# Kernel tuning notes

Hardware: AMD Instinct MI355X
Metric: run time of the kernel (lower is better)

The kernel has to match this reference:

```python
import jax, jax.numpy as jnp
import numpy as np

NH = 12      # bert-base heads
NL = 32      # num_latents
K = 64       # hard-coded topk in forward


def _ln(x, g, b):
    m = x.mean(-1, keepdims=True)
    v = ((x - m) ** 2).mean(-1, keepdims=True)
    return (x - m) / jnp.sqrt(v + 1e-12) * g + b


def _attn(xq, xkv, w, b, mask_add=None):
    # w: [4,H,H] (q,k,v,o), b: [4,H]
    B, Lq, H = xq.shape
    dh = H // NH
    q = (xq @ w[0] + b[0]).reshape(B, Lq, NH, dh)
    k = (xkv @ w[1] + b[1]).reshape(B, -1, NH, dh)
    v = (xkv @ w[2] + b[2]).reshape(B, -1, NH, dh)
    s = jnp.einsum('bqhd,bkhd->bhqk', q, k) / np.sqrt(dh).astype(xq.dtype)
    if mask_add is not None:
        s = s + mask_add
    p = jax.nn.softmax(s, axis=-1)          # [B,NH,Lq,Lk]
    o = jnp.einsum('bhqk,bkhd->bqhd', p, v).reshape(B, Lq, H)
    return o @ w[3] + b[3], p


def _cross_block(q, enc, w, b, g, lb, mask_add=None):
    # w:[L,8,H,H]; per layer: self-attn+LN then cross-attn+LN (FFN stripped)
    p_last = None
    for l in range(w.shape[0]):
        a, _ = _attn(q, q, w[l, :4], b[l, :4])
        q = _ln(q + a, g[l, 0], lb[l, 0])
        a, p_last = _attn(q, enc, w[l, 4:], b[l, 4:], mask_add)
        q = _ln(q + a, g[l, 1], lb[l, 1])
    return q, p_last


def _self_block(q, w, b, g, lb):
    probs = []
    for l in range(w.shape[0]):
        a, p = _attn(q, q, w[l], b[l])
        q = _ln(q + a, g[l, 0], lb[l, 0])
        probs.append(p)
    return q, jnp.concatenate(probs, axis=1)  # concat over head dim like torch.concat(attentions, dim=1)


def setup_inputs() -> dict:
    key = jax.random.key(0)
    ks = jax.random.split(key, 24)
    B, S, T, H, L = 32, 1024, 64, 768, 2
    std = 0.02
    inp = {
        'audio_embeds': jax.random.normal(ks[0], (B, S, H), jnp.float32),
        'text_embeds': jax.random.normal(ks[1], (B, T, H), jnp.float32),
        'attention_mask': jnp.ones((B, T), jnp.int32),
        'audio_qt': jax.random.normal(ks[2], (1, NL, H), jnp.float32) * std,
        'text_qt': jax.random.normal(ks[3], (1, NL, H), jnp.float32) * std,
    }
    for i, pre in enumerate(['tm', 'am', 'mg']):
        inp[pre + '_w'] = jax.random.normal(ks[4 + i], (L, 8, H, H), jnp.float32) * std
        inp[pre + '_b'] = jnp.zeros((L, 8, H), jnp.float32)
        inp[pre + '_g'] = jnp.ones((L, 2, H), jnp.float32)
        inp[pre + '_lb'] = jnp.zeros((L, 2, H), jnp.float32)
    inp['sel_w'] = jax.random.normal(ks[8], (L, 4, H, H), jnp.float32) * std
    inp['sel_b'] = jnp.zeros((L, 4, H), jnp.float32)
    inp['sel_g'] = jnp.ones((L, 1, H), jnp.float32)
    inp['sel_lb'] = jnp.zeros((L, 1, H), jnp.float32)
    return inp


def reference(audio_embeds, text_embeds, audio_qt, text_qt,
              tm_w, tm_b, tm_g, tm_lb, am_w, am_b, am_g, am_lb,
              sel_w, sel_b, sel_g, sel_lb, mg_w, mg_b, mg_g, mg_lb,
              attention_mask):
    B, S, H = audio_embeds.shape
    mask_add = (1.0 - attention_mask.astype(audio_embeds.dtype))[:, None, None, :] * -1e4

    # text token merger
    latent_text, _ = _cross_block(jnp.broadcast_to(text_qt, (B, NL, H)), text_embeds,
                                  tm_w, tm_b, tm_g, tm_lb, mask_add)
    # audio token merger (capture last-layer cross-attn probs)
    latent_audio, cross_p = _cross_block(jnp.broadcast_to(audio_qt, (B, NL, H)), audio_embeds,
                                         am_w, am_b, am_g, am_lb)
    latent_attention_score = cross_p.mean(axis=1)          # [B,NL,S]

    latent = jnp.concatenate([latent_audio, latent_text], axis=1)  # [B,2NL,H]
    fused, attn_all = _self_block(latent, sel_w, sel_b, sel_g, sel_lb)  # attn_all [B,L*NH,2NL,2NL]
    aas = attn_all[:, :, :NL, NL:].mean(axis=1)            # [B,NL,NL]

    imp = jnp.einsum('bqk,bks->bqs', aas, latent_attention_score).mean(axis=1)  # [B,S]
    _, idx = jax.lax.top_k(imp, K)
    sorted_idx = jnp.sort(idx, axis=1)                     # [B,K]

    sel_mask = jnp.zeros((B, S), bool).at[jnp.arange(B)[:, None], sorted_idx].set(True)
    q_tokens = jnp.take_along_axis(audio_embeds, sorted_idx[..., None], axis=1)  # [B,K,H]
    unsel_idx = jnp.argsort(sel_mask, axis=1, stable=True)[:, :S - K]            # order-preserving
    kv_rest = jnp.take_along_axis(audio_embeds, unsel_idx[..., None], axis=1)    # [B,S-K,H]
    kv = jnp.concatenate([kv_rest, fused], axis=1)                               # [B,S,H]

    out, _ = _cross_block(q_tokens, kv, mg_w, mg_b, mg_g, mg_lb)
    return out
```

## Files before the change

kernel.cpp:

```cpp
#include <hip/hip_runtime.h>
#include <hip/hip_bf16.h>
#include <math.h>

namespace {
constexpr int kB = 32, kS = 1024, kT = 64, kH = 768, kNH = 12, kDH = 64;
constexpr int kNL = 32, kTopK = 64, kL = 2;
constexpr size_t kMat = (size_t)kH * kH;
}

typedef _Float16 half8 __attribute__((ext_vector_type(8)));
typedef float floatx4 __attribute__((ext_vector_type(4)));

#define AS1U(p) ((const __attribute__((address_space(1))) unsigned int*)(p))
#define AS3U(p) ((__attribute__((address_space(3))) unsigned int*)(p))

__device__ __forceinline__ void split_write(float v, _Float16* H, _Float16* L, size_t i) {
    _Float16 h = (_Float16)v;
    H[i] = h;
    L[i] = (_Float16)(v - (float)h);
}

template<int NP>
__global__ __launch_bounds__(256) void gemm16x(
    const _Float16* __restrict__ Ah_, const _Float16* __restrict__ Al_,
    const _Float16* __restrict__ Bh_, const _Float16* __restrict__ Bl_,
    const float* __restrict__ bias,
    _Float16* __restrict__ Oh, _Float16* __restrict__ Ol, int M)
{
    const int nwg = gridDim.x;
    const int bid = blockIdx.x;
    const int cpx = nwg >> 3;
    const int swz = (bid & 7) * cpx + (bid >> 3);
    const int xn = swz % 6;
    const int ym = swz / 6;
    if (ym * 128 >= M) return;

    constexpr int NPL = (NP == 3) ? 4 : 2;
    __shared__ _Float16 lds[NPL * 4096];
    const int tid = threadIdx.x;
    const int lane = tid & 63, wave = tid >> 6;
    const size_t rm = (size_t)ym * 128;
    const size_t cn = (size_t)xn * 128;
    const int wr = (wave >> 1) * 64, wc = (wave & 1) * 64;

    const int lrow = lane >> 2;
    const int lchunk = (lane & 3) ^ ((lane >> 3) & 3);
    const int q = lane >> 4;
    const int fr = lane & 15;
    const int rslot = q ^ ((fr >> 1) & 3);

    const _Float16* gsrc;
    _Float16* lbase;
    int jbase;
    if constexpr (NP == 3) {
        gsrc = (wave == 0) ? Ah_ + rm * kH : (wave == 1) ? Al_ + rm * kH
             : (wave == 2) ? Bh_ + cn * kH : Bl_ + cn * kH;
        lbase = &lds[wave * 4096];
        jbase = 0;
    } else {
        gsrc = (wave < 2) ? Ah_ + rm * kH : Bh_ + cn * kH;
        lbase = &lds[(wave >> 1) * 4096];
        jbase = (wave & 1) * 4;
    }
    constexpr int CPW = (NP == 3) ? 8 : 4;

    floatx4 acc[4][4] = {};
    for (int k0 = 0; k0 < kH; k0 += 32) {
        #pragma unroll
        for (int c = 0; c < CPW; ++c) {
            int j = jbase + c;
            const _Float16* src = gsrc + (size_t)(j * 16 + lrow) * kH + k0 + lchunk * 8;
            _Float16* dst = lbase + j * 512 + lane * 8;
            __builtin_amdgcn_global_load_lds(AS1U(src), AS3U(dst), 16, 0, 0);
        }
        __syncthreads();
        half8 ah[4], bh[4], al[4], bl[4];
        #pragma unroll
        for (int m = 0; m < 4; ++m) {
            int r = wr + m * 16 + fr;
            ah[m] = *(const half8*)&lds[r * 32 + rslot * 8];
            if constexpr (NP == 3) al[m] = *(const half8*)&lds[4096 + r * 32 + rslot * 8];
        }
        constexpr int pb = (NP == 3) ? 2 : 1;
        #pragma unroll
        for (int n = 0; n < 4; ++n) {
            int r = wc + n * 16 + fr;
            bh[n] = *(const half8*)&lds[pb * 4096 + r * 32 + rslot * 8];
            if constexpr (NP == 3) bl[n] = *(const half8*)&lds[3 * 4096 + r * 32 + rslot * 8];
        }
        #pragma unroll
        for (int m = 0; m < 4; ++m)
            #pragma unroll
            for (int n = 0; n < 4; ++n) {
                acc[m][n] = __builtin_amdgcn_mfma_f32_16x16x32_f16(ah[m], bh[n], acc[m][n], 0, 0, 0);
                if constexpr (NP == 3) {
                    acc[m][n] = __builtin_amdgcn_mfma_f32_16x16x32_f16(ah[m], bl[n], acc[m][n], 0, 0, 0);
                    acc[m][n] = __builtin_amdgcn_mfma_f32_16x16x32_f16(al[m], bh[n], acc[m][n], 0, 0, 0);
                }
            }
        __syncthreads();
    }
    #pragma unroll
    for (int m = 0; m < 4; ++m) {
        int row0 = wr + m * 16 + (lane >> 4) * 4;
        #pragma unroll
        for (int n = 0; n < 4; ++n) {
            int col = (int)cn + wc + n * 16 + fr;
            float bv = bias[col];
            #pragma unroll
            for (int j = 0; j < 4; ++j) {
                float v = acc[m][n][j] + bv;
                size_t oi = (rm + row0 + j) * (size_t)kH + col;
                _Float16 hh = (_Float16)v;
                Oh[oi] = hh;
                if constexpr (NP == 3) Ol[oi] = (_Float16)(v - (float)hh);
            }
        }
    }
}

template<int NP>
__global__ __launch_bounds__(256) void gemm16s(
    const _Float16* __restrict__ Aqh, const _Float16* __restrict__ Aql,
    const _Float16* __restrict__ Aeh, const _Float16* __restrict__ Ael,
    const _Float16* __restrict__ Whb, const _Float16* __restrict__ Wlb,
    const float* __restrict__ bias,
    _Float16* __restrict__ O0h, _Float16* __restrict__ O0l,
    _Float16* __restrict__ O1h, _Float16* __restrict__ O1l,
    _Float16* __restrict__ O2h, _Float16* __restrict__ O2l,
    int Mq, int Mk)
{
    const int z = blockIdx.z;
    const int M = (z == 0) ? Mq : Mk;
    if ((int)blockIdx.x * 64 >= M) return;
    const _Float16* Ah = (z == 0) ? Aqh : Aeh;
    const _Float16* Al = (z == 0) ? Aql : Ael;
    const _Float16* Bh = Whb + (size_t)z * kMat;
    const _Float16* Bl = Wlb + (size_t)z * kMat;
    const float* bz = bias + z * kH;
    _Float16* Oh = (z == 0) ? O0h : (z == 1) ? O1h : O2h;
    _Float16* Ol = (z == 0) ? O0l : (z == 1) ? O1l : O2l;

    constexpr int NPL = (NP == 3) ? 4 : 2;
    __shared__ _Float16 lds[NPL * 2048];
    const int tid = threadIdx.x;
    const int lane = tid & 63, wave = tid >> 6;
    const size_t rm = (size_t)blockIdx.x * 64;
    const size_t cn = (size_t)blockIdx.y * 64;
    const int wr = (wave >> 1) * 32, wc = (wave & 1) * 32;

    const int lrow = lane >> 2;
    const int lchunk = (lane & 3) ^ ((lane >> 3) & 3);
    const int q = lane >> 4;
    const int fr = lane & 15;
    const int rslot = q ^ ((fr >> 1) & 3);

    const _Float16* gsrc;
    _Float16* lbase;
    int jbase;
    if constexpr (NP == 3) {
        gsrc = (wave == 0) ? Ah + rm * kH : (wave == 1) ? Al + rm * kH
             : (wave == 2) ? Bh + cn * kH : Bl + cn * kH;
        lbase = &lds[wave * 2048];
        jbase = 0;
    } else {
        gsrc = (wave < 2) ? Ah + rm * kH : Bh + cn * kH;
        lbase = &lds[(wave >> 1) * 2048];
        jbase = (wave & 1) * 2;
    }
    constexpr int CPW = (NP == 3) ? 4 : 2;

    floatx4 acc[2][2] = {};
    for (int k0 = 0; k0 < kH; k0 += 32) {
        #pragma unroll
        for (int c = 0; c < CPW; ++c) {
            int j = jbase + c;
            const _Float16* src = gsrc + (size_t)(j * 16 + lrow) * kH + k0 + lchunk * 8;
            _Float16* dst = lbase + j * 512 + lane * 8;
            __builtin_amdgcn_global_load_lds(AS1U(src), AS3U(dst), 16, 0, 0);
        }
        __syncthreads();
        half8 ah[2], bh[2], al[2], bl[2];
        #pragma unroll
        for (int m = 0; m < 2; ++m) {
            int r = wr + m * 16 + fr;
            ah[m] = *(const half8*)&lds[r * 32 + rslot * 8];
            if constexpr (NP == 3) al[m] = *(const half8*)&lds[2048 + r * 32 + rslot * 8];
        }
        constexpr int pb = (NP == 3) ? 2 : 1;
        #pragma unroll
        for (int n = 0; n < 2; ++n) {
            int r = wc + n * 16 + fr;
            bh[n] = *(const half8*)&lds[pb * 2048 + r * 32 + rslot * 8];
            if constexpr (NP == 3) bl[n] = *(const half8*)&lds[3 * 2048 + r * 32 + rslot * 8];
        }
        #pragma unroll
        for (int m = 0; m < 2; ++m)
            #pragma unroll
            for (int n = 0; n < 2; ++n) {
                acc[m][n] = __builtin_amdgcn_mfma_f32_16x16x32_f16(ah[m], bh[n], acc[m][n], 0, 0, 0);
                if constexpr (NP == 3) {
                    acc[m][n] = __builtin_amdgcn_mfma_f32_16x16x32_f16(ah[m], bl[n], acc[m][n], 0, 0, 0);
                    acc[m][n] = __builtin_amdgcn_mfma_f32_16x16x32_f16(al[m], bh[n], acc[m][n], 0, 0, 0);
                }
            }
        __syncthreads();
    }
    #pragma unroll
    for (int m = 0; m < 2; ++m) {
        int row0 = wr + m * 16 + (lane >> 4) * 4;
        #pragma unroll
        for (int n = 0; n < 2; ++n) {
            int col = (int)cn + wc + n * 16 + fr;
            float bv = bz[col];
            #pragma unroll
            for (int j = 0; j < 4; ++j) {
                float v = acc[m][n][j] + bv;
                size_t oi = (rm + row0 + j) * (size_t)kH + col;
                _Float16 hh = (_Float16)v;
                Oh[oi] = hh;
                if constexpr (NP == 3) Ol[oi] = (_Float16)(v - (float)hh);
            }
        }
    }
}

template<int NP>
__global__ __launch_bounds__(256) void gemm_o32s(
    const _Float16* __restrict__ Ah_, const _Float16* __restrict__ Al_,
    const _Float16* __restrict__ Bh_, const _Float16* __restrict__ Bl_,
    const float* __restrict__ bias, float* __restrict__ Y, int M)
{
    constexpr int NPL = (NP == 3) ? 4 : 2;
    __shared__ _Float16 lds[NPL * 2048];
    const int tid = threadIdx.x;
    const int lane = tid & 63, wave = tid >> 6;
    const size_t rm = (size_t)blockIdx.x * 64;
    const size_t cn = (size_t)blockIdx.y * 64;
    const int wr = (wave >> 1) * 32, wc = (wave & 1) * 32;

    const int lrow = lane >> 2;
    const int lchunk = (lane & 3) ^ ((lane >> 3) & 3);
    const int q = lane >> 4;
    const int fr = lane & 15;
    const int rslot = q ^ ((fr >> 1) & 3);

    const _Float16* gsrc;
    _Float16* lbase;
    int jbase;
    if constexpr (NP == 3) {
        gsrc = (wave == 0) ? Ah_ + rm * kH : (wave == 1) ? Al_ + rm * kH
             : (wave == 2) ? Bh_ + cn * kH : Bl_ + cn * kH;
        lbase = &lds[wave * 2048];
        jbase = 0;
    } else {
        gsrc = (wave < 2) ? Ah_ + rm * kH : Bh_ + cn * kH;
        lbase = &lds[(wave >> 1) * 2048];
        jbase = (wave & 1) * 2;
    }
    constexpr int CPW = (NP == 3) ? 4 : 2;

    floatx4 acc[2][2] = {};
    for (int k0 = 0; k0 < kH; k0 += 32) {
        #pragma unroll
        for (int c = 0; c < CPW; ++c) {
            int j = jbase + c;
            const _Float16* src = gsrc + (size_t)(j * 16 + lrow) * kH + k0 + lchunk * 8;
            _Float16* dst = lbase + j * 512 + lane * 8;
            __builtin_amdgcn_global_load_lds(AS1U(src), AS3U(dst), 16, 0, 0);
        }
        __syncthreads();
        half8 ah[2], bh[2], al[2], bl[2];
        #pragma unroll
        for (int m = 0; m < 2; ++m) {
            int r = wr + m * 16 + fr;
            ah[m] = *(const half8*)&lds[r * 32 + rslot * 8];
            if constexpr (NP == 3) al[m] = *(const half8*)&lds[2048 + r * 32 + rslot * 8];
        }
        constexpr int pb = (NP == 3) ? 2 : 1;
        #pragma unroll
        for (int n = 0; n < 2; ++n) {
            int r = wc + n * 16 + fr;
            bh[n] = *(const half8*)&lds[pb * 2048 + r * 32 + rslot * 8];
            if constexpr (NP == 3) bl[n] = *(const half8*)&lds[3 * 2048 + r * 32 + rslot * 8];
        }
        #pragma unroll
        for (int m = 0; m < 2; ++m)
            #pragma unroll
            for (int n = 0; n < 2; ++n) {
                acc[m][n] = __builtin_amdgcn_mfma_f32_16x16x32_f16(ah[m], bh[n], acc[m][n], 0, 0, 0);
                if constexpr (NP == 3) {
                    acc[m][n] = __builtin_amdgcn_mfma_f32_16x16x32_f16(ah[m], bl[n], acc[m][n], 0, 0, 0);
                    acc[m][n] = __builtin_amdgcn_mfma_f32_16x16x32_f16(al[m], bh[n], acc[m][n], 0, 0, 0);
                }
            }
        __syncthreads();
    }
    #pragma unroll
    for (int m = 0; m < 2; ++m) {
        int row0 = wr + m * 16 + (lane >> 4) * 4;
        #pragma unroll
        for (int n = 0; n < 2; ++n) {
            int col = (int)cn + wc + n * 16 + fr;
            float bv = bias[col];
            #pragma unroll
            for (int j = 0; j < 4; ++j)
                Y[(rm + row0 + j) * (size_t)kH + col] = acc[m][n][j] + bv;
        }
    }
}

template<int NP>
__global__ __launch_bounds__(256) void attn_big(
    const _Float16* __restrict__ Qh, const _Float16* __restrict__ Ql,
    const _Float16* __restrict__ Kh, const _Float16* __restrict__ Kl,
    float* __restrict__ P, int Lq, int Lk)
{
    constexpr int NPL = (NP == 3) ? 2 : 1;
    const int tid = threadIdx.x, lane = tid & 63, wave = tid >> 6;
    const int fr = lane & 15, part = lane >> 4;
    const int bh = blockIdx.x, b = bh / kNH, h = bh % kNH;
    const int q0 = blockIdx.y * 32;
    const int key0 = wave * 256;
    __shared__ float red[32][4];

    half8 qa[2][2][NPL];
    #pragma unroll
    for (int m = 0; m < 2; ++m)
        #pragma unroll
        for (int c = 0; c < 2; ++c) {
            size_t ro = (size_t)(b * Lq + q0 + m * 16 + fr) * kH + h * kDH + c * 32 + part * 8;
            qa[m][c][0] = *(const half8*)&Qh[ro];
            if constexpr (NP == 3) qa[m][c][1] = *(const half8*)&Ql[ro];
        }
    floatx4 acc[2][16] = {};
    #pragma unroll
    for (int n = 0; n < 16; ++n)
        #pragma unroll
        for (int c = 0; c < 2; ++c) {
            size_t ro = (size_t)(b * Lk + key0 + n * 16 + fr) * kH + h * kDH + c * 32 + part * 8;
            half8 kh8 = *(const half8*)&Kh[ro];
            half8 kl8;
            if constexpr (NP == 3) kl8 = *(const half8*)&Kl[ro];
            #pragma unroll
            for (int m = 0; m < 2; ++m) {
                acc[m][n] = __builtin_amdgcn_mfma_f32_16x16x32_f16(qa[m][c][0], kh8, acc[m][n], 0, 0, 0);
                if constexpr (NP == 3) {
                    acc[m][n] = __builtin_amdgcn_mfma_f32_16x16x32_f16(qa[m][c][0], kl8, acc[m][n], 0, 0, 0);
                    acc[m][n] = __builtin_amdgcn_mfma_f32_16x16x32_f16(qa[m][c][1], kh8, acc[m][n], 0, 0, 0);
                }
            }
        }
    #pragma unroll
    for (int m = 0; m < 2; ++m)
        #pragma unroll
        for (int n = 0; n < 16; ++n)
            #pragma unroll
            for (int j = 0; j < 4; ++j) acc[m][n][j] *= 0.125f;
    #pragma unroll
    for (int m = 0; m < 2; ++m)
        #pragma unroll
        for (int j = 0; j < 4; ++j) {
            float v = acc[m][0][j];
            #pragma unroll
            for (int n = 1; n < 16; ++n) v = fmaxf(v, acc[m][n][j]);
            #pragma unroll
            for (int o = 1; o < 16; o <<= 1) v = fmaxf(v, __shfl_xor(v, o));
            red[m * 16 + part * 4 + j][wave] = v;
        }
    __syncthreads();
    float gm[2][4];
    #pragma unroll
    for (int m = 0; m < 2; ++m)
        #pragma unroll
        for (int j = 0; j < 4; ++j) {
            int r = m * 16 + part * 4 + j;
            gm[m][j] = fmaxf(fmaxf(red[r][0], red[r][1]), fmaxf(red[r][2], red[r][3]));
        }
    __syncthreads();
    #pragma unroll
    for (int m = 0; m < 2; ++m)
        #pragma unroll
        for (int j = 0; j < 4; ++j) {
            float s = 0.f;
            #pragma unroll
            for (int n = 0; n < 16; ++n) {
                float e = expf(acc[m][n][j] - gm[m][j]);
                acc[m][n][j] = e;
                s += e;
            }
            #pragma unroll
            for (int o = 1; o < 16; o <<= 1) s += __shfl_xor(s, o);
            red[m * 16 + part * 4 + j][wave] = s;
        }
    __syncthreads();
    #pragma unroll
    for (int m = 0; m < 2; ++m)
        #pragma unroll
        for (int j = 0; j < 4; ++j) {
            int r = m * 16 + part * 4 + j;
            float inv = 1.0f / (red[r][0] + red[r][1] + red[r][2] + red[r][3]);
            size_t rowbase = ((size_t)bh * Lq + q0 + m * 16 + part * 4 + j) * Lk + key0;
            #pragma unroll
            for (int n = 0; n < 16; ++n)
                P[rowbase + n * 16 + fr] = acc[m][n][j] * inv;
        }
}

template<int LQ, int NP>
__global__ __launch_bounds__((LQ / 16) * 64) void pv_mfma(
    const float* __restrict__ P,
    const _Float16* __restrict__ Vh, const _Float16* __restrict__ Vl,
    _Float16* __restrict__ Oh, _Float16* __restrict__ Ol, int Lk)
{
    constexpr int NW = LQ / 16, NT = NW * 64;
    constexpr int NPL = (NP == 3) ? 2 : 1;
    __shared__ _Float16 vT[NPL][64][72];
    const int tid = threadIdx.x, lane = tid & 63, wave = tid >> 6;
    const int fr = lane & 15, part = lane >> 4;
    const int bh = blockIdx.x, b = bh / kNH, h = bh % kNH;
    const int qbase = wave * 16;

    floatx4 acc[4] = {};
    for (int kb = 0; kb < Lk; kb += 64) {
        for (int idx = tid; idx < 64 * 8; idx += NT) {
            int r = idx >> 3, c8 = idx & 7;
            half8 v = *(const half8*)&Vh[(size_t)(b * Lk + kb + r) * kH + h * kDH + c8 * 8];
            #pragma unroll
            for (int e = 0; e < 8; ++e) vT[0][c8 * 8 + e][r] = v[e];
            if constexpr (NP == 3) {
                half8 w = *(const half8*)&Vl[(size_t)(b * Lk + kb + r) * kH + h * kDH + c8 * 8];
                #pragma unroll
                for (int e = 0; e < 8; ++e) vT[1][c8 * 8 + e][r] = w[e];
            }
        }
        __syncthreads();
        half8 pa[2][NPL];
        #pragma unroll
        for (int c = 0; c < 2; ++c) {
            const float* src = &P[((size_t)bh * LQ + qbase + fr) * Lk + kb + c * 32 + part * 8];
            float4 x = *(const float4*)src, y = *(const float4*)(src + 4);
            float vv[8] = {x.x, x.y, x.z, x.w, y.x, y.y, y.z, y.w};
            #pragma unroll
            for (int e = 0; e < 8; ++e) {
                _Float16 hh = (_Float16)vv[e];
                pa[c][0][e] = hh;
                if constexpr (NP == 3) pa[c][1][e] = (_Float16)(vv[e] - (float)hh);
            }
        }
        #pragma unroll
        for (int n = 0; n < 4; ++n)
            #pragma unroll
            for (int c = 0; c < 2; ++c) {
                half8 bh8 = *(const half8*)&vT[0][n * 16 + fr][c * 32 + part * 8];
                acc[n] = __builtin_amdgcn_mfma_f32_16x16x32_f16(pa[c][0], bh8, acc[n], 0, 0, 0);
                if constexpr (NP == 3) {
                    half8 bl8 = *(const half8*)&vT[1][n * 16 + fr][c * 32 + part * 8];
                    acc[n] = __builtin_amdgcn_mfma_f32_16x16x32_f16(pa[c][0], bl8, acc[n], 0, 0, 0);
                    acc[n] = __builtin_amdgcn_mfma_f32_16x16x32_f16(pa[c][1], bh8, acc[n], 0, 0, 0);
                }
            }
        __syncthreads();
    }
    #pragma unroll
    for (int n = 0; n < 4; ++n)
        #pragma unroll
        for (int j = 0; j < 4; ++j) {
            size_t oi = (size_t)(b * LQ + qbase + part * 4 + j) * kH + h * kDH + n * 16 + fr;
            float v = acc[n][j];
            _Float16 hh = (_Float16)v;
            Oh[oi] = hh;
            if constexpr (NP == 3) Ol[oi] = (_Float16)(v - (float)hh);
        }
}

template<int LQ, int LK, int NP, bool MASKED, bool CAPTURE>
__global__ __launch_bounds__((LQ / 16) * 64) void attn_small(
    const _Float16* Qh, const _Float16* Ql,
    const _Float16* __restrict__ Kh, const _Float16* __restrict__ Kl,
    const _Float16* __restrict__ Vh, const _Float16* __restrict__ Vl,
    _Float16* Oh, _Float16* Ol,
    float* __restrict__ Pcap, const int* __restrict__ amask)
{
    constexpr int NW = LQ / 16, NT = NW * 64, NN = LK / 16, NC = LK / 32;
    constexpr int NPL = (NP == 3) ? 2 : 1;
    constexpr int PIT = LK + 8;
    __shared__ _Float16 vT[NPL][64][PIT];
    __shared__ _Float16 Pld[NW][NPL][16][PIT];
    const int tid = threadIdx.x, lane = tid & 63, wave = tid >> 6;
    const int fr = lane & 15, part = lane >> 4;
    const int bh = blockIdx.x, b = bh / kNH, h = bh % kNH;

    for (int idx = tid; idx < LK * 8; idx += NT) {
        int r = idx >> 3, c8 = idx & 7;
        half8 v = *(const half8*)&Vh[(size_t)(b * LK + r) * kH + h * kDH + c8 * 8];
        #pragma unroll
        for (int e = 0; e < 8; ++e) vT[0][c8 * 8 + e][r] = v[e];
        if constexpr (NP == 3) {
            half8 w = *(const half8*)&Vl[(size_t)(b * LK + r) * kH + h * kDH + c8 * 8];
            #pragma unroll
            for (int e = 0; e < 8; ++e) vT[1][c8 * 8 + e][r] = w[e];
        }
    }
    half8 qa[2][NPL];
    #pragma unroll
    for (int c = 0; c < 2; ++c) {
        size_t ro = (size_t)(b * LQ + wave * 16 + fr) * kH + h * kDH + c * 32 + part * 8;
        qa[c][0] = *(const half8*)&Qh[ro];
        if constexpr (NP == 3) qa[c][1] = *(const half8*)&Ql[ro];
    }
    floatx4 acc[NN] = {};
    #pragma unroll
    for (int n = 0; n < NN; ++n)
        #pragma unroll
        for (int c = 0; c < 2; ++c) {
            size_t ro = (size_t)(b * LK + n * 16 + fr) * kH + h * kDH + c * 32 + part * 8;
            half8 kh8 = *(const half8*)&Kh[ro];
            acc[n] = __builtin_amdgcn_mfma_f32_16x16x32_f16(qa[c][0], kh8, acc[n], 0, 0, 0);
            if constexpr (NP == 3) {
                half8 kl8 = *(const half8*)&Kl[ro];
                acc[n] = __builtin_amdgcn_mfma_f32_16x16x32_f16(qa[c][0], kl8, acc[n], 0, 0, 0);
                acc[n] = __builtin_amdgcn_mfma_f32_16x16x32_f16(qa[c][1], kh8, acc[n], 0, 0, 0);
            }
        }
    #pragma unroll
    for (int n = 0; n < NN; ++n) {
        float madd = 0.f;
        if constexpr (MASKED)
            madd = (1.0f - (float)amask[b * kT + n * 16 + fr]) * -1e4f;
        #pragma unroll
        for (int j = 0; j < 4; ++j) acc[n][j] = acc[n][j] * 0.125f + madd;
    }
    #pragma unroll
    for (int j = 0; j < 4; ++j) {
        float m = acc[0][j];
        #pragma unroll
        for (int n = 1; n < NN; ++n) m = fmaxf(m, acc[n][j]);
        #pragma unroll
        for (int o = 1; o < 16; o <<= 1) m = fmaxf(m, __shfl_xor(m, o));
        float s = 0.f;
        #pragma unroll
        for (int n = 0; n < NN; ++n) { float e = expf(acc[n][j] - m); acc[n][j] = e; s += e; }
        #pragma unroll
        for (int o = 1; o < 16; o <<= 1) s += __shfl_xor(s, o);
        float inv = 1.0f / s;
        #pragma unroll
        for (int n = 0; n < NN; ++n) acc[n][j] *= inv;
    }
    #pragma unroll
    for (int n = 0; n < NN; ++n)
        #pragma unroll
        for (int j = 0; j < 4; ++j) {
            float p = acc[n][j];
            if constexpr (CAPTURE)
                Pcap[((size_t)bh * LQ + wave * 16 + part * 4 + j) * LK + n * 16 + fr] = p;
            _Float16 ph = (_Float16)p;
            Pld[wave][0][part * 4 + j][n * 16 + fr] = ph;
            if constexpr (NP == 3)
                Pld[wave][1][part * 4 + j][n * 16 + fr] = (_Float16)(p - (float)ph);
        }
    __syncthreads();
    floatx4 o4[4] = {};
    #pragma unroll
    for (int n = 0; n < 4; ++n)
        #pragma unroll
        for (int c = 0; c < NC; ++c) {
            half8 ph8 = *(const half8*)&Pld[wave][0][fr][c * 32 + part * 8];
            half8 vh8 = *(const half8*)&vT[0][n * 16 + fr][c * 32 + part * 8];
            o4[n] = __builtin_amdgcn_mfma_f32_16x16x32_f16(ph8, vh8, o4[n], 0, 0, 0);
            if constexpr (NP == 3) {
                half8 pl8 = *(const half8*)&Pld[wave][1][fr][c * 32 + part * 8];
                half8 vl8 = *(const half8*)&vT[1][n * 16 + fr][c * 32 + part * 8];
                o4[n] = __builtin_amdgcn_mfma_f32_16x16x32_f16(ph8, vl8, o4[n], 0, 0, 0);
                o4[n] = __builtin_amdgcn_mfma_f32_16x16x32_f16(pl8, vh8, o4[n], 0, 0, 0);
            }
        }
    #pragma unroll
    for (int n = 0; n < 4; ++n)
        #pragma unroll
        for (int j = 0; j < 4; ++j) {
            size_t oi = (size_t)(b * LQ + wave * 16 + part * 4 + j) * kH + h * kDH + n * 16 + fr;
            float v = o4[n][j];
            _Float16 hh = (_Float16)v;
            Oh[oi] = hh;
            if constexpr (NP == 3) Ol[oi] = (_Float16)(v - (float)hh);
        }
}

__global__ __launch_bounds__(256) void wconv(const float* __restrict__ W,
    _Float16* __restrict__ Th, _Float16* __restrict__ Tl)
{
    __shared__ float t[32][33];
    const int mat = blockIdx.z;
    const int k0 = blockIdx.y * 32, n0 = blockIdx.x * 32;
    const int tid = threadIdx.x;
    #pragma unroll
    for (int i = 0; i < 4; ++i) {
        int e = tid + i * 256, r = e >> 5, c = e & 31;
        t[r][c] = W[(size_t)mat * kMat + (size_t)(k0 + r) * kH + n0 + c];
    }
    __syncthreads();
    #pragma unroll
    for (int i = 0; i < 4; ++i) {
        int e = tid + i * 256, r = e >> 5, c = e & 31;
        float v = t[c][r];
        split_write(v, Th, Tl, (size_t)mat * kMat + (size_t)(n0 + r) * kH + k0 + c);
    }
}

__global__ __launch_bounds__(256) void split2(const float* __restrict__ X,
    _Float16* __restrict__ H, _Float16* __restrict__ L, int n)
{
    int i = (blockIdx.x * 256 + threadIdx.x) * 4;
    if (i >= n) return;
    float4 v = *(const float4*)&X[i];
    split_write(v.x, H, L, i);
    split_write(v.y, H, L, i + 1);
    split_write(v.z, H, L, i + 2);
    split_write(v.w, H, L, i + 3);
}

__global__ __launch_bounds__(256) void ln_residual(const float* __restrict__ X,
    const float* __restrict__ A, const float* __restrict__ g,
    const float* __restrict__ lb, float* __restrict__ Y,
    _Float16* __restrict__ Yh, _Float16* __restrict__ Yl)
{
    const size_t row = blockIdx.x;
    const int tid = threadIdx.x;
    __shared__ float red[4];
    float x[3];
    float sum = 0.f;
    #pragma unroll
    for (int i = 0; i < 3; ++i) {
        int c = tid + i * 256;
        x[i] = X[row * kH + c] + A[row * kH + c];
        sum += x[i];
    }
    for (int o = 32; o > 0; o >>= 1) sum += __shfl_xor(sum, o);
    if ((tid & 63) == 0) red[tid >> 6] = sum;
    __syncthreads();
    sum = red[0] + red[1] + red[2] + red[3];
    float mean = sum * (1.0f / 768.0f);
    float vs = 0.f;
    #pragma unroll
    for (int i = 0; i < 3; ++i) { float d = x[i] - mean; vs += d * d; }
    for (int o = 32; o > 0; o >>= 1) vs += __shfl_xor(vs, o);
    __syncthreads();
    if ((tid & 63) == 0) red[tid >> 6] = vs;
    __syncthreads();
    vs = red[0] + red[1] + red[2] + red[3];
    float inv = 1.0f / sqrtf(vs * (1.0f / 768.0f) + 1e-12f);
    #pragma unroll
    for (int i = 0; i < 3; ++i) {
        int c = tid + i * 256;
        float y = (x[i] - mean) * inv * g[c] + lb[c];
        Y[row * kH + c] = y;
        if (Yh) split_write(y, Yh, Yl, row * kH + c);
    }
}

__global__ __launch_bounds__(256) void mean_heads(const float* __restrict__ P,
    float* __restrict__ out)
{
    const int bq = blockIdx.x;
    const int b = bq / kNL, q = bq % kNL;
    for (int s = threadIdx.x; s < kS; s += 256) {
        float acc = 0.f;
        for (int h = 0; h < kNH; ++h)
            acc += P[((size_t)(b * kNH + h) * kNL + q) * kS + s];
        out[(size_t)bq * kS + s] = acc * (1.0f / kNH);
    }
}

__global__ __launch_bounds__(256) void aas_acc(const float* __restrict__ P,
    float* __restrict__ aas, int init)
{
    const int b = blockIdx.x;
    for (int idx = threadIdx.x; idx < kNL * kNL; idx += 256) {
        int q = idx >> 5, k = idx & 31;
        float acc = 0.f;
        for (int h = 0; h < kNH; ++h)
            acc += P[((size_t)(b * kNH + h) * 64 + q) * 64 + 32 + k];
        size_t o = (size_t)b * kNL * kNL + idx;
        if (init) aas[o] = acc; else aas[o] += acc;
    }
}

__global__ __launch_bounds__(256) void imp_kernel(const float* __restrict__ aas,
    const float* __restrict__ score, float* __restrict__ imp)
{
    const int b = blockIdx.x;
    __shared__ float w[kNL];
    if (threadIdx.x < kNL) {
        float acc = 0.f;
        for (int q = 0; q < kNL; ++q)
            acc += aas[((size_t)b * kNL + q) * kNL + threadIdx.x];
        w[threadIdx.x] = acc;
    }
    __syncthreads();
    for (int s = threadIdx.x; s < kS; s += 256) {
        float acc = 0.f;
        for (int k = 0; k < kNL; ++k)
            acc += w[k] * score[((size_t)b * kNL + k) * kS + s];
        imp[(size_t)b * kS + s] = acc;
    }
}

__global__ __launch_bounds__(256) void topk_kernel(const float* __restrict__ imp,
    int* __restrict__ selidx, int* __restrict__ unselidx)
{
    const int b = blockIdx.x;
    const int tid = threadIdx.x;
    __shared__ unsigned long long keys[kS];
    __shared__ int wsum[4];
    for (int i = tid; i < kS; i += 256) {
        unsigned u = __float_as_uint(imp[(size_t)b * kS + i]);
        u = (u & 0x80000000u) ? ~u : (u | 0x80000000u);
        keys[i] = ((unsigned long long)u << 32) | (unsigned)(kS - 1 - i);
    }
    __syncthreads();
    unsigned long long me[4];
    int r[4] = {0, 0, 0, 0};
    #pragma unroll
    for (int j = 0; j < 4; ++j) me[j] = keys[tid * 4 + j];
    for (int t = 0; t < kS; ++t) {
        unsigned long long k = keys[t];
        #pragma unroll
        for (int j = 0; j < 4; ++j) r[j] += (k > me[j]) ? 1 : 0;
    }
    int flag[4], cnt = 0;
    #pragma unroll
    for (int j = 0; j < 4; ++j) { flag[j] = (r[j] < kTopK); cnt += flag[j]; }
    const int lane = tid & 63, w = tid >> 6;
    int incl = cnt;
    for (int o = 1; o < 64; o <<= 1) {
        int t = __shfl_up(incl, o);
        if (lane >= o) incl += t;
    }
    if (lane == 63) wsum[w] = incl;
    __syncthreads();
    int wbase = 0;
    for (int i = 0; i < w; ++i) wbase += wsum[i];
    int sbase = wbase + incl - cnt;
    int ubase = tid * 4 - sbase;
    #pragma unroll
    for (int j = 0; j < 4; ++j) {
        int i = tid * 4 + j;
        if (flag[j]) selidx[b * kTopK + sbase++] = i;
        else         unselidx[b * (kS - kTopK) + ubase++] = i;
    }
}

__global__ __launch_bounds__(256) void bcast_q(const float* __restrict__ qt,
    float* __restrict__ q, _Float16* __restrict__ Qh, _Float16* __restrict__ Ql)
{
    const int bn = blockIdx.x;
    const int n = bn & (kNL - 1);
    for (int c = threadIdx.x; c < kH; c += 256) {
        float v = qt[(size_t)n * kH + c];
        q[(size_t)bn * kH + c] = v;
        split_write(v, Qh, Ql, (size_t)bn * kH + c);
    }
}

__global__ __launch_bounds__(256) void concat_lat(const float* __restrict__ qa,
    const float* __restrict__ qt, float* __restrict__ lat,
    _Float16* __restrict__ Lh, _Float16* __restrict__ Ll)
{
    const int br = blockIdx.x;
    const int b = br >> 6, r = br & 63;
    const float* src = (r < kNL) ? qa + (size_t)(b * kNL + r) * kH
                                 : qt + (size_t)(b * kNL + (r - kNL)) * kH;
    for (int c = threadIdx.x; c < kH; c += 256) {
        float v = src[c];
        lat[(size_t)br * kH + c] = v;
        split_write(v, Lh, Ll, (size_t)br * kH + c);
    }
}

__global__ __launch_bounds__(256) void gather_q(const float* __restrict__ audio,
    const int* __restrict__ selidx, float* __restrict__ qm,
    _Float16* __restrict__ Qh, _Float16* __restrict__ Ql)
{
    const int bj = blockIdx.x;
    const int b = bj >> 6;
    const int srow = selidx[bj];
    const float* src = audio + ((size_t)b * kS + srow) * kH;
    for (int c = threadIdx.x; c < kH; c += 256) {
        float v = src[c];
        qm[(size_t)bj * kH + c] = v;
        split_write(v, Qh, Ql, (size_t)bj * kH + c);
    }
}

__global__ __launch_bounds__(256) void build_kv(const float* __restrict__ audio,
    const float* __restrict__ fused, const int* __restrict__ unselidx,
    _Float16* __restrict__ Kh, _Float16* __restrict__ Kl)
{
    const int br = blockIdx.x;
    const int b = br >> 10, r = br & 1023;
    const float* src;
    if (r < kS - kTopK) src = audio + ((size_t)b * kS + unselidx[b * (kS - kTopK) + r]) * kH;
    else                src = fused + (size_t)(b * kTopK + (r - (kS - kTopK))) * kH;
    for (int c = threadIdx.x; c < kH; c += 256)
        split_write(src[c], Kh, Kl, (size_t)br * kH + c);
}

extern "C" void kernel_launch(void* const* d_in, const int* in_sizes, int n_in,
                              void* d_out, int out_size, void* d_ws, size_t ws_size,
                              hipStream_t stream)
{
    const float* audio    = (const float*)d_in[0];
    const float* text     = (const float*)d_in[1];
    const int*   amask    = (const int*)  d_in[2];
    const float* audio_qt = (const float*)d_in[3];
    const float* text_qt  = (const float*)d_in[4];
    const float* tm_w  = (const float*)d_in[5];
    const float* tm_b  = (const float*)d_in[6];
    const float* tm_g  = (const float*)d_in[7];
    const float* tm_lb = (const float*)d_in[8];
    const float* am_w  = (const float*)d_in[9];
    const float* am_b  = (const float*)d_in[10];
    const float* am_g  = (const float*)d_in[11];
    const float* am_lb = (const float*)d_in[12];
    const float* mg_w  = (const float*)d_in[13];
    const float* mg_b  = (const float*)d_in[14];
    const float* mg_g  = (const float*)d_in[15];
    const float* mg_lb = (const float*)d_in[16];
    const float* sel_w  = (const float*)d_in[17];
    const float* sel_b  = (const float*)d_in[18];
    const float* sel_g  = (const float*)d_in[19];
    const float* sel_lb = (const float*)d_in[20];
    (void)in_sizes; (void)n_in; (void)out_size;

    char* base = (char*)d_ws;
    size_t off = 0;
    auto A = [&](size_t bytes) {
        off = (off + 255) & ~(size_t)255;
        void* p = base + off; off += bytes; return p;
    };
    float* Pbuf   = (float*)A((size_t)kB * kNH * 64 * kS * 4);
    float* attA   = (float*)A((size_t)2048 * kH * 4);
    float* q_text = (float*)A((size_t)1024 * kH * 4);
    float* q_audio= (float*)A((size_t)1024 * kH * 4);
    float* latent = (float*)A((size_t)2048 * kH * 4);
    float* qmerge = (float*)A((size_t)2048 * kH * 4);
    float* latsc  = (float*)A((size_t)kB * kNL * kS * 4);
    float* aas    = (float*)A((size_t)kB * kNL * kNL * 4);
    float* impb   = (float*)A((size_t)kB * kS * 4);
    int* selidx   = (int*)A((size_t)kB * kTopK * 4);
    int* unselidx = (int*)A((size_t)kB * (kS - kTopK) * 4);
    _Float16* Wh  = (_Float16*)A(8 * kMat * 2);
    _Float16* Wl  = (_Float16*)A(8 * kMat * 2);
    _Float16* BGh = (_Float16*)A((size_t)kB * kS * kH * 2);
    _Float16* BGl = (_Float16*)A((size_t)kB * kS * kH * 2);
    _Float16* PTh = (_Float16*)A((size_t)kB * kT * kH * 2);
    _Float16* PTl = (_Float16*)A((size_t)kB * kT * kH * 2);
    _Float16* PLqh= (_Float16*)A((size_t)2048 * kH * 2);
    _Float16* PLql= (_Float16*)A((size_t)2048 * kH * 2);
    _Float16* PLoh= (_Float16*)A((size_t)2048 * kH * 2);
    _Float16* PLol= (_Float16*)A((size_t)2048 * kH * 2);
    _Float16* KVh = (_Float16*)A((size_t)kB * kS * kH * 2);
    _Float16* KVl = (_Float16*)A((size_t)kB * kS * kH * 2);
    if (off > ws_size) return;

    _Float16* Qh = PLoh;
    _Float16* Ql = PLol;

    auto attn = [&](const float* qf, int Lq,
                    const _Float16* qah, const _Float16* qal,
                    const _Float16* eah, const _Float16* eal, int Lk,
                    int wmat, const float* bias, const float* g, const float* lb,
                    const int* mask, int capture, bool np3,
                    float* q_out, _Float16* oh, _Float16* ol)
    {
        const int Mq = kB * Lq, Mk = kB * Lk;
        const _Float16* WhB = Wh + (size_t)wmat * kMat;
        const _Float16* WlB = Wl + (size_t)wmat * kMat;
        if (Lk >= 256) {
            dim3 gq(Mq / 64, 12, 1);
            if (np3) gemm16s<3><<<gq, 256, 0, stream>>>(qah, qal, qah, qal, WhB, WlB, bias,
                         Qh, Ql, nullptr, nullptr, nullptr, nullptr, Mq, Mq);
            else     gemm16s<1><<<gq, 256, 0, stream>>>(qah, qal, qah, qal, WhB, WlB, bias,
                         Qh, Ql, nullptr, nullptr, nullptr, nullptr, Mq, Mq);
            const int nwgK = 6 * (Mk / 128);
            if (np3) gemm16x<3><<<nwgK, 256, 0, stream>>>(eah, eal, WhB + 1 * kMat, WlB + 1 * kMat,
                         bias + 1 * kH, KVh, KVl, Mk);
            else     gemm16x<1><<<nwgK, 256, 0, stream>>>(eah, eal, WhB + 1 * kMat, WlB + 1 * kMat,
                         bias + 1 * kH, KVh, KVl, Mk);
            dim3 g2(kB * kNH, Lq / 32);
            if (np3) attn_big<3><<<g2, 256, 0, stream>>>(Qh, Ql, KVh, KVl, Pbuf, Lq, Lk);
            else     attn_big<1><<<g2, 256, 0, stream>>>(Qh, Ql, KVh, KVl, Pbuf, Lq, Lk);
            if (capture == 1) mean_heads<<<kB * kNL, 256, 0, stream>>>(Pbuf, latsc);
            if (np3) gemm16x<3><<<nwgK, 256, 0, stream>>>(eah, eal, WhB + 2 * kMat, WlB + 2 * kMat,
                         bias + 2 * kH, KVh, KVl, Mk);
            else     gemm16x<1><<<nwgK, 256, 0, stream>>>(eah, eal, WhB + 2 * kMat, WlB + 2 * kMat,
                         bias + 2 * kH, KVh, KVl, Mk);
            if (Lq == 32) {
                if (np3) pv_mfma<32, 3><<<kB * kNH, 128, 0, stream>>>(Pbuf, KVh, KVl, PLoh, PLol, Lk);
                else     pv_mfma<32, 1><<<kB * kNH, 128, 0, stream>>>(Pbuf, KVh, KVl, PLoh, PLol, Lk);
            } else {
                if (np3) pv_mfma<64, 3><<<kB * kNH, 256, 0, stream>>>(Pbuf, KVh, KVl, PLoh, PLol, Lk);
                else     pv_mfma<64, 1><<<kB * kNH, 256, 0, stream>>>(Pbuf, KVh, KVl, PLoh, PLol, Lk);
            }
        } else {
            _Float16* V2h = KVh + (size_t)Mk * kH;
            _Float16* V2l = KVl + (size_t)Mk * kH;
            const int gx = (Mq > Mk ? Mq : Mk) / 64;
            dim3 g1(gx, 12, 3);
            if (np3) gemm16s<3><<<g1, 256, 0, stream>>>(qah, qal, eah, eal, WhB, WlB, bias,
                         Qh, Ql, KVh, KVl, V2h, V2l, Mq, Mk);
            else     gemm16s<1><<<g1, 256, 0, stream>>>(qah, qal, eah, eal, WhB, WlB, bias,
                         Qh, Ql, KVh, KVl, V2h, V2l, Mq, Mk);
            if (Lq == 32 && Lk == 32)
                attn_small<32, 32, 3, false, false><<<kB * kNH, 128, 0, stream>>>(
                    Qh, Ql, KVh, KVl, V2h, V2l, PLoh, PLol, nullptr, nullptr);
            else if (Lq == 32 && Lk == 64)
                attn_small<32, 64, 3, true, false><<<kB * kNH, 128, 0, stream>>>(
                    Qh, Ql, KVh, KVl, V2h, V2l, PLoh, PLol, nullptr, mask);
            else if (np3)
                attn_small<64, 64, 3, false, true><<<kB * kNH, 256, 0, stream>>>(
                    Qh, Ql, KVh, KVl, V2h, V2l, PLoh, PLol, Pbuf, nullptr);
            else
                attn_small<64, 64, 1, false, false><<<kB * kNH, 256, 0, stream>>>(
                    Qh, Ql, KVh, KVl, V2h, V2l, PLoh, PLol, nullptr, nullptr);
            if (capture == 2)      aas_acc<<<kB, 256, 0, stream>>>(Pbuf, aas, 1);
            else if (capture == 3) aas_acc<<<kB, 256, 0, stream>>>(Pbuf, aas, 0);
        }
        dim3 g4(Mq / 64, 12);
        if (np3) gemm_o32s<3><<<g4, 256, 0, stream>>>(PLoh, PLol, WhB + 3 * kMat, WlB + 3 * kMat,
                     bias + 3 * kH, attA, Mq);
        else     gemm_o32s<1><<<g4, 256, 0, stream>>>(PLoh, PLol, WhB + 3 * kMat, WlB + 3 * kMat,
                     bias + 3 * kH, attA, Mq);
        ln_residual<<<Mq, 256, 0, stream>>>(qf, attA, g, lb, q_out, oh, ol);
    };

    split2<<<(kB * kT * kH) / 1024, 256, 0, stream>>>(text, PTh, PTl, kB * kT * kH);
    split2<<<(kB * kS * kH) / 1024, 256, 0, stream>>>(audio, BGh, BGl, kB * kS * kH);

    bcast_q<<<kB * kNL, 256, 0, stream>>>(text_qt, q_text, PLqh, PLql);
    for (int l = 0; l < kL; ++l) {
        wconv<<<dim3(24, 24, 8), 256, 0, stream>>>(tm_w + (size_t)l * 8 * kMat, Wh, Wl);
        attn(q_text, kNL, PLqh, PLql, PLqh, PLql, kNL, 0,
             tm_b + (size_t)l * 8 * kH, tm_g + (size_t)l * 2 * kH, tm_lb + (size_t)l * 2 * kH,
             nullptr, 0, true, q_text, PLqh, PLql);
        attn(q_text, kNL, PLqh, PLql, PTh, PTl, kT, 4,
             tm_b + ((size_t)l * 8 + 4) * kH, tm_g + ((size_t)l * 2 + 1) * kH, tm_lb + ((size_t)l * 2 + 1) * kH,
             amask, 0, true, q_text, PLqh, PLql);
    }
    bcast_q<<<kB * kNL, 256, 0, stream>>>(audio_qt, q_audio, PLqh, PLql);
    for (int l = 0; l < kL; ++l) {
        wconv<<<dim3(24, 24, 8), 256, 0, stream>>>(am_w + (size_t)l * 8 * kMat, Wh, Wl);
        attn(q_audio, kNL, PLqh, PLql, PLqh, PLql, kNL, 0,
             am_b + (size_t)l * 8 * kH, am_g + (size_t)l * 2 * kH, am_lb + (size_t)l * 2 * kH,
             nullptr, 0, true, q_audio, PLqh, PLql);
        attn(q_audio, kNL, PLqh, PLql, BGh, BGl, kS, 4,
             am_b + ((size_t)l * 8 + 4) * kH, am_g + ((size_t)l * 2 + 1) * kH, am_lb + ((size_t)l * 2 + 1) * kH,
             nullptr, (l == kL - 1) ? 1 : 0, true, q_audio, PLqh, PLql);
    }
    concat_lat<<<kB * 64, 256, 0, stream>>>(q_audio, q_text, latent, PLqh, PLql);
    for (int l = 0; l < kL; ++l) {
        wconv<<<dim3(24, 24, 4), 256, 0, stream>>>(sel_w + (size_t)l * 4 * kMat, Wh, Wl);
        attn(latent, 64, PLqh, PLql, PLqh, PLql, 64, 0,
             sel_b + (size_t)l * 4 * kH, sel_g + (size_t)l * kH, sel_lb + (size_t)l * kH,
             nullptr, (l == 0) ? 2 : 3, true, latent, PLqh, PLql);
    }
    imp_kernel<<<kB, 256, 0, stream>>>(aas, latsc, impb);
    topk_kernel<<<kB, 256, 0, stream>>>(impb, selidx, unselidx);
    gather_q<<<kB * kTopK, 256, 0, stream>>>(audio, selidx, qmerge, PLqh, PLql);
    build_kv<<<kB * kS, 256, 0, stream>>>(audio, latent, unselidx, BGh, BGl);
    for (int l = 0; l < kL; ++l) {
        wconv<<<dim3(24, 24, 8), 256, 0, stream>>>(mg_w + (size_t)l * 8 * kMat, Wh, Wl);
        attn(qmerge, 64, PLqh, PLql, PLqh, PLql, 64, 0,
             mg_b + (size_t)l * 8 * kH, mg_g + (size_t)l * 2 * kH, mg_lb + (size_t)l * 2 * kH,
             nullptr, 0, false, qmerge, PLqh, PLql);
        float* qo = (l == kL - 1) ? (float*)d_out : qmerge;
        _Float16* oh = (l == kL - 1) ? nullptr : PLqh;
        _Float16* ol = (l == kL - 1) ? nullptr : PLql;
        attn(qmerge, 64, PLqh, PLql, BGh, BGl, kS, 4,
             mg_b + ((size_t)l * 8 + 4) * kH, mg_g + ((size_t)l * 2 + 1) * kH, mg_lb + ((size_t)l * 2 + 1) * kH,
             nullptr, 0, false, qo, oh, ol);
    }
}
```

Before: 2.088 ms.

## Double-buffer LDS tiles in GEMM kernels to overlap loads with MFMA

The three split-fp16 GEMM kernels now keep two LDS buffers. Each iteration issues the global-to-LDS copy for the next K tile before running the MFMAs on the current one, and the trailing barrier per iteration is removed. The aim is to hide global memory latency behind the matrix math and to halve the barrier count. In exchange, LDS use per block doubles (64KB for the large 3-plane variant), which can lower occupancy.

Measured after the change: 2.016 ms (median of 2 runs). 3.4% less time.

```diff
diff --git a/kernel.cpp b/kernel.cpp
--- a/kernel.cpp
+++ b/kernel.cpp
@@ -36,7 +36,7 @@
     if (ym * 128 >= M) return;
 
     constexpr int NPL = (NP == 3) ? 4 : 2;
-    __shared__ _Float16 lds[NPL * 4096];
+    __shared__ _Float16 lds[2][NPL * 4096];
     const int tid = threadIdx.x;
     const int lane = tid & 63, wave = tid >> 6;
     const size_t rm = (size_t)ym * 128;
@@ -50,43 +50,50 @@
     const int rslot = q ^ ((fr >> 1) & 3);
 
     const _Float16* gsrc;
-    _Float16* lbase;
-    int jbase;
+    int lplane, jbase;
     if constexpr (NP == 3) {
         gsrc = (wave == 0) ? Ah_ + rm * kH : (wave == 1) ? Al_ + rm * kH
              : (wave == 2) ? Bh_ + cn * kH : Bl_ + cn * kH;
-        lbase = &lds[wave * 4096];
+        lplane = wave;
         jbase = 0;
     } else {
         gsrc = (wave < 2) ? Ah_ + rm * kH : Bh_ + cn * kH;
-        lbase = &lds[(wave >> 1) * 4096];
+        lplane = wave >> 1;
         jbase = (wave & 1) * 4;
     }
     constexpr int CPW = (NP == 3) ? 8 : 4;
 
-    floatx4 acc[4][4] = {};
-    for (int k0 = 0; k0 < kH; k0 += 32) {
+    auto stage = [&](int buf, int k0) {
         #pragma unroll
         for (int c = 0; c < CPW; ++c) {
             int j = jbase + c;
             const _Float16* src = gsrc + (size_t)(j * 16 + lrow) * kH + k0 + lchunk * 8;
-            _Float16* dst = lbase + j * 512 + lane * 8;
+            _Float16* dst = &lds[buf][lplane * 4096 + j * 512 + lane * 8];
             __builtin_amdgcn_global_load_lds(AS1U(src), AS3U(dst), 16, 0, 0);
         }
+    };
+
+    floatx4 acc[4][4] = {};
+    int cur = 0;
+    stage(0, 0);
+    constexpr int NT = kH / 32;
+    for (int kt = 0; kt < NT; ++kt) {
         __syncthreads();
+        if (kt + 1 < NT) stage(cur ^ 1, (kt + 1) * 32);
+        const _Float16* L = lds[cur];
         half8 ah[4], bh[4], al[4], bl[4];
         #pragma unroll
         for (int m = 0; m < 4; ++m) {
             int r = wr + m * 16 + fr;
-            ah[m] = *(const half8*)&lds[r * 32 + rslot * 8];
-            if constexpr (NP == 3) al[m] = *(const half8*)&lds[4096 + r * 32 + rslot * 8];
+            ah[m] = *(const half8*)&L[r * 32 + rslot * 8];
+            if constexpr (NP == 3) al[m] = *(const half8*)&L[4096 + r * 32 + rslot * 8];
         }
         constexpr int pb = (NP == 3) ? 2 : 1;
         #pragma unroll
         for (int n = 0; n < 4; ++n) {
             int r = wc + n * 16 + fr;
-            bh[n] = *(const half8*)&lds[pb * 4096 + r * 32 + rslot * 8];
-            if constexpr (NP == 3) bl[n] = *(const half8*)&lds[3 * 4096 + r * 32 + rslot * 8];
+            bh[n] = *(const half8*)&L[pb * 4096 + r * 32 + rslot * 8];
+            if constexpr (NP == 3) bl[n] = *(const half8*)&L[3 * 4096 + r * 32 + rslot * 8];
         }
         #pragma unroll
         for (int m = 0; m < 4; ++m)
@@ -98,7 +105,7 @@
                     acc[m][n] = __builtin_amdgcn_mfma_f32_16x16x32_f16(al[m], bh[n], acc[m][n], 0, 0, 0);
                 }
             }
-        __syncthreads();
+        cur ^= 1;
     }
     #pragma unroll
     for (int m = 0; m < 4; ++m) {
@@ -142,7 +149,7 @@
     _Float16* Ol = (z == 0) ? O0l : (z == 1) ? O1l : O2l;
 
     constexpr int NPL = (NP == 3) ? 4 : 2;
-    __shared__ _Float16 lds[NPL * 2048];
+    __shared__ _Float16 lds[2][NPL * 2048];
     const int tid = threadIdx.x;
     const int lane = tid & 63, wave = tid >> 6;
     const size_t rm = (size_t)blockIdx.x * 64;
@@ -156,43 +163,50 @@
     const int rslot = q ^ ((fr >> 1) & 3);
 
     const _Float16* gsrc;
-    _Float16* lbase;
-    int jbase;
+    int lplane, jbase;
     if constexpr (NP == 3) {
         gsrc = (wave == 0) ? Ah + rm * kH : (wave == 1) ? Al + rm * kH
              : (wave == 2) ? Bh + cn * kH : Bl + cn * kH;
-        lbase = &lds[wave * 2048];
+        lplane = wave;
         jbase = 0;
     } else {
         gsrc = (wave < 2) ? Ah + rm * kH : Bh + cn * kH;
-        lbase = &lds[(wave >> 1) * 2048];
+        lplane = wave >> 1;
         jbase = (wave & 1) * 2;
     }
     constexpr int CPW = (NP == 3) ? 4 : 2;
 
-    floatx4 acc[2][2] = {};
-    for (int k0 = 0; k0 < kH; k0 += 32) {
+    auto stage = [&](int buf, int k0) {
         #pragma unroll
         for (int c = 0; c < CPW; ++c) {
             int j = jbase + c;
             const _Float16* src = gsrc + (size_t)(j * 16 + lrow) * kH + k0 + lchunk * 8;
-            _Float16* dst = lbase + j * 512 + lane * 8;
+            _Float16* dst = &lds[buf][lplane * 2048 + j * 512 + lane * 8];
             __builtin_amdgcn_global_load_lds(AS1U(src), AS3U(dst), 16, 0, 0);
         }
+    };
+
+    floatx4 acc[2][2] = {};
+    int cur = 0;
+    stage(0, 0);
+    constexpr int NT = kH / 32;
+    for (int kt = 0; kt < NT; ++kt) {
         __syncthreads();
+        if (kt + 1 < NT) stage(cur ^ 1, (kt + 1) * 32);
+        const _Float16* L = lds[cur];
         half8 ah[2], bh[2], al[2], bl[2];
         #pragma unroll
         for (int m = 0; m < 2; ++m) {
             int r = wr + m * 16 + fr;
-            ah[m] = *(const half8*)&lds[r * 32 + rslot * 8];
-            if constexpr (NP == 3) al[m] = *(const half8*)&lds[2048 + r * 32 + rslot * 8];
+            ah[m] = *(const half8*)&L[r * 32 + rslot * 8];
+            if constexpr (NP == 3) al[m] = *(const half8*)&L[2048 + r * 32 + rslot * 8];
         }
         constexpr int pb = (NP == 3) ? 2 : 1;
         #pragma unroll
         for (int n = 0; n < 2; ++n) {
             int r = wc + n * 16 + fr;
-            bh[n] = *(const half8*)&lds[pb * 2048 + r * 32 + rslot * 8];
-            if constexpr (NP == 3) bl[n] = *(const half8*)&lds[3 * 2048 + r * 32 + rslot * 8];
+            bh[n] = *(const half8*)&L[pb * 2048 + r * 32 + rslot * 8];
+            if constexpr (NP == 3) bl[n] = *(const half8*)&L[3 * 2048 + r * 32 + rslot * 8];
         }
         #pragma unroll
         for (int m = 0; m < 2; ++m)
@@ -204,7 +218,7 @@
                     acc[m][n] = __builtin_amdgcn_mfma_f32_16x16x32_f16(al[m], bh[n], acc[m][n], 0, 0, 0);
                 }
             }
-        __syncthreads();
+        cur ^= 1;
     }
     #pragma unroll
     for (int m = 0; m < 2; ++m) {
@@ -232,7 +246,7 @@
     const float* __restrict__ bias, float* __restrict__ Y, int M)
 {
     constexpr int NPL = (NP == 3) ? 4 : 2;
-    __shared__ _Float16 lds[NPL * 2048];
+    __shared__ _Float16 lds[2][NPL * 2048];
     const int tid = threadIdx.x;
     const int lane = tid & 63, wave = tid >> 6;
     const size_t rm = (size_t)blockIdx.x * 64;
@@ -246,43 +260,50 @@
     const int rslot = q ^ ((fr >> 1) & 3);
 
     const _Float16* gsrc;
-    _Float16* lbase;
-    int jbase;
+    int lplane, jbase;
     if constexpr (NP == 3) {
         gsrc = (wave == 0) ? Ah_ + rm * kH : (wave == 1) ? Al_ + rm * kH
              : (wave == 2) ? Bh_ + cn * kH : Bl_ + cn * kH;
-        lbase = &lds[wave * 2048];
+        lplane = wave;
         jbase = 0;
     } else {
         gsrc = (wave < 2) ? Ah_ + rm * kH : Bh_ + cn * kH;
-        lbase = &lds[(wave >> 1) * 2048];
+        lplane = wave >> 1;
         jbase = (wave & 1) * 2;
     }
     constexpr int CPW = (NP == 3) ? 4 : 2;
 
-    floatx4 acc[2][2] = {};
-    for (int k0 = 0; k0 < kH; k0 += 32) {
+    auto stage = [&](int buf, int k0) {
         #pragma unroll
         for (int c = 0; c < CPW; ++c) {
             int j = jbase + c;
             const _Float16* src = gsrc + (size_t)(j * 16 + lrow) * kH + k0 + lchunk * 8;
-            _Float16* dst = lbase + j * 512 + lane * 8;
+            _Float16* dst = &lds[buf][lplane * 2048 + j * 512 + lane * 8];
             __builtin_amdgcn_global_load_lds(AS1U(src), AS3U(dst), 16, 0, 0);
         }
+    };
+
+    floatx4 acc[2][2] = {};
+    int cur = 0;
+    stage(0, 0);
+    constexpr int NT = kH / 32;
+    for (int kt = 0; kt < NT; ++kt) {
         __syncthreads();
+        if (kt + 1 < NT) stage(cur ^ 1, (kt + 1) * 32);
+        const _Float16* L = lds[cur];
         half8 ah[2], bh[2], al[2], bl[2];
         #pragma unroll
         for (int m = 0; m < 2; ++m) {
             int r = wr + m * 16 + fr;
-            ah[m] = *(const half8*)&lds[r * 32 + rslot * 8];
-            if constexpr (NP == 3) al[m] = *(const half8*)&lds[2048 + r * 32 + rslot * 8];
+            ah[m] = *(const half8*)&L[r * 32 + rslot * 8];
+            if constexpr (NP == 3) al[m] = *(const half8*)&L[2048 + r * 32 + rslot * 8];
         }
         constexpr int pb = (NP == 3) ? 2 : 1;
         #pragma unroll
         for (int n = 0; n < 2; ++n) {
             int r = wc + n * 16 + fr;
-            bh[n] = *(const half8*)&lds[pb * 2048 + r * 32 + rslot * 8];
-            if constexpr (NP == 3) bl[n] = *(const half8*)&lds[3 * 2048 + r * 32 + rslot * 8];
+            bh[n] = *(const half8*)&L[pb * 2048 + r * 32 + rslot * 8];
+            if constexpr (NP == 3) bl[n] = *(const half8*)&L[3 * 2048 + r * 32 + rslot * 8];
         }
         #pragma unroll
         for (int m = 0; m < 2; ++m)
@@ -294,7 +315,7 @@
                     acc[m][n] = __builtin_amdgcn_mfma_f32_16x16x32_f16(al[m], bh[n], acc[m][n], 0, 0, 0);
                 }
             }
-        __syncthreads();
+        cur ^= 1;
     }
     #pragma unroll
     for (int m = 0; m < 2; ++m) {
```
